# Kernel tuning notes

Measured on AMD Instinct MI355X. Metric: run time of the kernel, lower is better.

## Reference

```python
import jax, jax.numpy as jnp
import numpy as np

N, E, IN, H, K = 50000, 800000, 64, 64, 16


def _linear_params(key, fan_in, fan_out):
    kw, kb = jax.random.split(key)
    lim = 1.0 / np.sqrt(fan_in)
    W = jax.random.uniform(kw, (fan_in, fan_out), jnp.float32, -lim, lim)
    b = jax.random.uniform(kb, (fan_out,), jnp.float32, -lim, lim)
    return W, b


def setup_inputs() -> dict:
    key = jax.random.key(0)
    ks = jax.random.split(key, 16)
    x = jax.random.normal(ks[0], (N, IN), jnp.float32)
    edge_index = jax.random.randint(ks[1], (2, E), 0, N, jnp.int64)
    edge_attr = jax.random.uniform(ks[2], (E, 1), jnp.float32)
    curr_idx = jax.random.randint(ks[3], (), 0, N, jnp.int64)
    dest_idx = jax.random.randint(ks[4], (), 0, N, jnp.int64)
    neighbor_indices = jax.random.randint(ks[5], (K,), 0, N, jnp.int64)
    # GINEConv1 params: edge lift Linear(1->IN), mlp1 Linear(IN->H), Linear(H->H)
    We1, be1 = _linear_params(ks[6], 1, IN)
    W1a, b1a = _linear_params(ks[7], IN, H)
    W1b, b1b = _linear_params(ks[8], H, H)
    # GINEConv2 params: edge lift Linear(1->H), mlp2 Linear(H->H), Linear(H->H)
    We2, be2 = _linear_params(ks[9], 1, H)
    W2a, b2a = _linear_params(ks[10], H, H)
    W2b, b2b = _linear_params(ks[11], H, H)
    # Q head: lin1 Linear(3H->H), lin2 Linear(H->1)
    Wl1, bl1 = _linear_params(ks[12], 3 * H, H)
    Wl2, bl2 = _linear_params(ks[13], H, 1)
    return dict(x=x, edge_index=edge_index, curr_idx=curr_idx, dest_idx=dest_idx,
                neighbor_indices=neighbor_indices, edge_attr=edge_attr,
                We1=We1, be1=be1, W1a=W1a, b1a=b1a, W1b=W1b, b1b=b1b,
                We2=We2, be2=be2, W2a=W2a, b2a=b2a, W2b=W2b, b2b=b2b,
                Wl1=Wl1, bl1=bl1, Wl2=Wl2, bl2=bl2)


def _gine(x, src, dst, e_emb, Wa, ba, Wb, bb):
    # message = ReLU(x_j + edge_emb); aggregate = sum over incoming edges; eps = 0
    msg = jax.nn.relu(x[src] + e_emb)                      # [E, d]
    agg = jax.ops.segment_sum(msg, dst, num_segments=x.shape[0])  # [N, d]
    h = x + agg                                            # (1+eps)*x + agg
    return jax.nn.relu(h @ Wa + ba) @ Wb + bb


def reference(x, edge_index, curr_idx, dest_idx, neighbor_indices, edge_attr,
              We1, be1, W1a, b1a, W1b, b1b,
              We2, be2, W2a, b2a, W2b, b2b,
              Wl1, bl1, Wl2, bl2):
    src, dst = edge_index[0], edge_index[1]
    h = _gine(x, src, dst, edge_attr @ We1 + be1, W1a, b1a, W1b, b1b)
    h = jax.nn.relu(h)
    h = _gine(h, src, dst, edge_attr @ We2 + be2, W2a, b2a, W2b, b2b)  # [N, H]
    curr = h[curr_idx]                 # [H]
    dest = h[dest_idx]                 # [H]
    nbr = h[neighbor_indices]          # [K, H]
    k = nbr.shape[0]
    cat = jnp.concatenate([jnp.broadcast_to(curr, (k, curr.shape[0])),
                           jnp.broadcast_to(dest, (k, dest.shape[0])),
                           nbr], axis=-1)                  # [K, 3H]
    q = jax.nn.relu(cat @ Wl1 + bl1) @ Wl2 + bl2           # [K, 1]
    return q[:, 0]
```

## Files before the change

kernel.cpp:

```cpp
#include <hip/hip_runtime.h>

#define NDIM 64
#define KNBR 16
#define NT 18
#define CAP_S1 1024
#define CAP_B1 128
#define CAP_B2 128

#define OFF_CNT   0
#define OFF_BC1   64
#define OFF_BC2   (OFF_BC1 + CAP_S1*4)
#define OFF_BM    (OFF_BC2 + 128)
#define ZERO_BYTES (OFF_BM + 2048*4)
#define OFF_TGT   ZERO_BYTES
#define OFF_S1    (OFF_TGT + 128)
#define OFF_B1    (OFF_S1 + CAP_S1*4)
#define OFF_B2    (OFF_B1 + CAP_S1*CAP_B1*4)
#define OFF_H     (OFF_B2 + 32*CAP_B2*4)
#define OFF_OUTH  (OFF_H + CAP_S1*NDIM*4)
#define OFF_SLOT  (OFF_OUTH + 32*NDIM*4)

__device__ __forceinline__ int imin(int a, int b) { return a < b ? a : b; }

__device__ __forceinline__ void claim_node(int v, int* slotOf, int* cnt,
                                           int* s1list, unsigned* bm) {
    int prev = atomicCAS(&slotOf[v], -1, -2);
    if (prev == -1) {
        int s = atomicAdd(&cnt[0], 1);
        if (s < CAP_S1) s1list[s] = v;
        __threadfence();
        slotOf[v] = s;
        atomicOr(&bm[v >> 5], 1u << (v & 31));
    }
}

__global__ void k_pass1(const int* __restrict__ src, const int* __restrict__ dst, int E,
                        const int* __restrict__ curr, const int* __restrict__ dest,
                        const int* __restrict__ nbr,
                        int* cnt, int* slotOf, int* s1list, unsigned* bm,
                        int* bc2, int* b2, int* tgt) {
    int t[NT];
    t[0] = curr[0];
    t[1] = dest[0];
    #pragma unroll
    for (int j = 0; j < KNBR; ++j) t[2 + j] = nbr[j];

    if (blockIdx.x == 0 && threadIdx.x < NT) {
        int id = t[threadIdx.x];
        tgt[threadIdx.x] = id;
        claim_node(id, slotOf, cnt, s1list, bm);
    }

    int i = blockIdx.x * blockDim.x + threadIdx.x;
    int e0 = i * 4;
    if (e0 >= E) return;
    int dv4[4];
    if (e0 + 3 < E) {
        int4 dv = ((const int4*)dst)[i];
        dv4[0] = dv.x; dv4[1] = dv.y; dv4[2] = dv.z; dv4[3] = dv.w;
    } else {
        #pragma unroll
        for (int j = 0; j < 4; ++j) dv4[j] = (e0 + j < E) ? dst[e0 + j] : -1;
    }
    #pragma unroll
    for (int j = 0; j < 4; ++j) {
        int d = dv4[j];
        bool any = false;
        #pragma unroll
        for (int k = 0; k < NT; ++k) {
            if (d == t[k]) {
                any = true;
                int idx = atomicAdd(&bc2[k], 1);
                if (idx < CAP_B2) b2[k * CAP_B2 + idx] = e0 + j;
            }
        }
        if (any) claim_node(src[e0 + j], slotOf, cnt, s1list, bm);
    }
}

__global__ void k_pass2(const int* __restrict__ dst, int E,
                        const unsigned* __restrict__ bm, const int* __restrict__ slotOf,
                        int* bc1, int* b1) {
    int i = blockIdx.x * blockDim.x + threadIdx.x;
    int e0 = i * 4;
    if (e0 >= E) return;
    int dv4[4];
    if (e0 + 3 < E) {
        int4 dv = ((const int4*)dst)[i];
        dv4[0] = dv.x; dv4[1] = dv.y; dv4[2] = dv.z; dv4[3] = dv.w;
    } else {
        #pragma unroll
        for (int j = 0; j < 4; ++j) dv4[j] = (e0 + j < E) ? dst[e0 + j] : -1;
    }
    #pragma unroll
    for (int j = 0; j < 4; ++j) {
        int d = dv4[j];
        if (d < 0) continue;
        if ((bm[d >> 5] >> (d & 31)) & 1u) {
            int s = slotOf[d];
            if (s >= 0 && s < CAP_S1) {
                int idx = atomicAdd(&bc1[s], 1);
                if (idx < CAP_B1) b1[s * CAP_B1 + idx] = e0 + j;
            }
        }
    }
}

__global__ void k_node1(const int* cnt, const int* __restrict__ s1list,
                        const int* __restrict__ bc1, const int* __restrict__ b1,
                        const int* __restrict__ src, const float* __restrict__ eattr,
                        const float* __restrict__ x,
                        const float* __restrict__ We1, const float* __restrict__ be1,
                        const float* __restrict__ W1a, const float* __restrict__ b1a,
                        const float* __restrict__ W1b, const float* __restrict__ b1b,
                        float* hbuf) {
    int s = blockIdx.x;
    if (s >= imin(cnt[0], CAP_S1)) return;
    int lane = threadIdx.x;
    __shared__ int   sv[CAP_B1];
    __shared__ float sa[CAP_B1];
    __shared__ float t[NDIM], u[NDIM];
    int m = imin(bc1[s], CAP_B1);
    for (int base = 0; base < m; base += NDIM) {
        int i = base + lane;
        if (i < m) {
            int e = b1[s * CAP_B1 + i];
            sv[i] = src[e];
            sa[i] = eattr[e];
        }
    }
    __syncthreads();
    float w = We1[lane], b = be1[lane];
    int v = s1list[s];
    float acc = x[(size_t)v * NDIM + lane];
    #pragma unroll 4
    for (int i = 0; i < m; ++i)
        acc += fmaxf(x[(size_t)sv[i] * NDIM + lane] + fmaf(sa[i], w, b), 0.f);
    t[lane] = acc;
    __syncthreads();
    float a1 = b1a[lane];
    #pragma unroll
    for (int k = 0; k < NDIM; ++k) a1 = fmaf(t[k], W1a[k * NDIM + lane], a1);
    u[lane] = fmaxf(a1, 0.f);
    __syncthreads();
    float a2 = b1b[lane];
    #pragma unroll
    for (int k = 0; k < NDIM; ++k) a2 = fmaf(u[k], W1b[k * NDIM + lane], a2);
    hbuf[(size_t)s * NDIM + lane] = fmaxf(a2, 0.f);
}

__global__ void k_mlp2(const int* __restrict__ tgt, const int* __restrict__ slotOf,
                       const int* __restrict__ bc2, const int* __restrict__ b2,
                       const int* __restrict__ src, const float* __restrict__ eattr,
                       const float* __restrict__ hbuf,
                       const float* __restrict__ We2, const float* __restrict__ be2,
                       const float* __restrict__ W2a, const float* __restrict__ b2a,
                       const float* __restrict__ W2b, const float* __restrict__ b2b,
                       float* outh) {
    int k = blockIdx.x;
    int lane = threadIdx.x;
    __shared__ int   ss[CAP_B2];
    __shared__ float sa[CAP_B2];
    __shared__ float t[NDIM], u[NDIM];
    int m = imin(bc2[k], CAP_B2);
    for (int base = 0; base < m; base += NDIM) {
        int i = base + lane;
        if (i < m) {
            int e = b2[k * CAP_B2 + i];
            ss[i] = slotOf[src[e]];
            sa[i] = eattr[e];
        }
    }
    __syncthreads();
    int sv = slotOf[tgt[k]];
    float acc = hbuf[(size_t)sv * NDIM + lane];
    float w2e = We2[lane], b2e = be2[lane];
    #pragma unroll 4
    for (int i = 0; i < m; ++i) {
        int s = ss[i];
        if (s >= 0 && s < CAP_S1)
            acc += fmaxf(hbuf[(size_t)s * NDIM + lane] + fmaf(sa[i], w2e, b2e), 0.f);
    }
    t[lane] = acc;
    __syncthreads();
    float a1 = b2a[lane];
    #pragma unroll
    for (int kk = 0; kk < NDIM; ++kk) a1 = fmaf(t[kk], W2a[kk * NDIM + lane], a1);
    u[lane] = fmaxf(a1, 0.f);
    __syncthreads();
    float a2 = b2b[lane];
    #pragma unroll
    for (int kk = 0; kk < NDIM; ++kk) a2 = fmaf(u[kk], W2b[kk * NDIM + lane], a2);
    outh[k * NDIM + lane] = a2;
}

__global__ void k_q(const float* __restrict__ outh,
                    const float* __restrict__ Wl1, const float* __restrict__ bl1,
                    const float* __restrict__ Wl2, const float* __restrict__ bl2,
                    float* out) {
    int j = blockIdx.x;
    int d = threadIdx.x;
    const float* c0 = outh;
    const float* c1 = outh + NDIM;
    const float* cn = outh + (2 + j) * NDIM;
    float acc = bl1[d];
    #pragma unroll
    for (int i = 0; i < NDIM; ++i) acc = fmaf(c0[i], Wl1[i * NDIM + d], acc);
    #pragma unroll
    for (int i = 0; i < NDIM; ++i) acc = fmaf(c1[i], Wl1[(NDIM + i) * NDIM + d], acc);
    #pragma unroll
    for (int i = 0; i < NDIM; ++i) acc = fmaf(cn[i], Wl1[(2 * NDIM + i) * NDIM + d], acc);
    acc = fmaxf(acc, 0.f) * Wl2[d];
    #pragma unroll
    for (int off = 32; off > 0; off >>= 1) acc += __shfl_down(acc, off);
    if (d == 0) out[j] = acc + bl2[0];
}

extern "C" void kernel_launch(void* const* d_in, const int* in_sizes, int n_in,
                              void* d_out, int out_size, void* d_ws, size_t ws_size,
                              hipStream_t stream) {
    const float* x     = (const float*)d_in[0];
    const int*   eidx  = (const int*)d_in[1];
    const int    E     = in_sizes[1] / 2;
    const int    Nn    = in_sizes[0] / NDIM;
    const int*   src   = eidx;
    const int*   dstA  = eidx + E;
    const int*   curr  = (const int*)d_in[2];
    const int*   dest  = (const int*)d_in[3];
    const int*   nbr   = (const int*)d_in[4];
    const float* eattr = (const float*)d_in[5];
    const float* We1 = (const float*)d_in[6];
    const float* be1 = (const float*)d_in[7];
    const float* W1a = (const float*)d_in[8];
    const float* b1a = (const float*)d_in[9];
    const float* W1b = (const float*)d_in[10];
    const float* b1b = (const float*)d_in[11];
    const float* We2 = (const float*)d_in[12];
    const float* be2 = (const float*)d_in[13];
    const float* W2a = (const float*)d_in[14];
    const float* b2a = (const float*)d_in[15];
    const float* W2b = (const float*)d_in[16];
    const float* b2b = (const float*)d_in[17];
    const float* Wl1 = (const float*)d_in[18];
    const float* bl1 = (const float*)d_in[19];
    const float* Wl2 = (const float*)d_in[20];
    const float* bl2 = (const float*)d_in[21];

    char* ws = (char*)d_ws;
    int*      cnt    = (int*)(ws + OFF_CNT);
    int*      bc1    = (int*)(ws + OFF_BC1);
    int*      bc2    = (int*)(ws + OFF_BC2);
    unsigned* bm     = (unsigned*)(ws + OFF_BM);
    int*      tgt    = (int*)(ws + OFF_TGT);
    int*      s1list = (int*)(ws + OFF_S1);
    int*      b1     = (int*)(ws + OFF_B1);
    int*      b2     = (int*)(ws + OFF_B2);
    float*    hbuf   = (float*)(ws + OFF_H);
    float*    outh   = (float*)(ws + OFF_OUTH);
    int*      slotOf = (int*)(ws + OFF_SLOT);

    hipMemsetAsync(ws, 0, ZERO_BYTES, stream);
    hipMemsetAsync(ws + OFF_SLOT, 0xFF, (size_t)Nn * 4, stream);

    int nQuad = (E + 3) / 4;
    int scanBlocks = (nQuad + 255) / 256;

    k_pass1<<<scanBlocks, 256, 0, stream>>>(src, dstA, E, curr, dest, nbr,
                                            cnt, slotOf, s1list, bm, bc2, b2, tgt);
    k_pass2<<<scanBlocks, 256, 0, stream>>>(dstA, E, bm, slotOf, bc1, b1);
    k_node1<<<CAP_S1, NDIM, 0, stream>>>(cnt, s1list, bc1, b1, src, eattr, x,
                                         We1, be1, W1a, b1a, W1b, b1b, hbuf);
    k_mlp2 <<<NT, NDIM, 0, stream>>>(tgt, slotOf, bc2, b2, src, eattr, hbuf,
                                     We2, be2, W2a, b2a, W2b, b2b, outh);
    k_q    <<<KNBR, NDIM, 0, stream>>>(outh, Wl1, bl1, Wl2, bl2, (float*)d_out);
}
```

Baseline: 151.2 us.

## Fuse all stages into one persistent kernel with software grid barriers

Replaces five kernel launches and two memsets with a single persistent kernel of 512 blocks that separates stages with atomic-counter grid barriers. Workspace initialisation moves into the kernel, and the destination indices are loaded once into registers and reused for both edge-scan passes instead of being read from memory twice. Node MLP work is mapped one wave per node, packing four nodes per block. The cost is a spin-wait barrier that assumes all 512 blocks are co-resident, and the final stages run on only a few blocks while the rest sit idle at barriers.

```diff
diff --git a/kernel.cpp b/kernel.cpp
--- a/kernel.cpp
+++ b/kernel.cpp
@@ -6,21 +6,35 @@
 #define CAP_S1 1024
 #define CAP_B1 128
 #define CAP_B2 128
-
-#define OFF_CNT   0
-#define OFF_BC1   64
-#define OFF_BC2   (OFF_BC1 + CAP_S1*4)
-#define OFF_BM    (OFF_BC2 + 128)
-#define ZERO_BYTES (OFF_BM + 2048*4)
-#define OFF_TGT   ZERO_BYTES
-#define OFF_S1    (OFF_TGT + 128)
-#define OFF_B1    (OFF_S1 + CAP_S1*4)
-#define OFF_B2    (OFF_B1 + CAP_S1*CAP_B1*4)
-#define OFF_H     (OFF_B2 + 32*CAP_B2*4)
-#define OFF_OUTH  (OFF_H + CAP_S1*NDIM*4)
-#define OFF_SLOT  (OFF_OUTH + 32*NDIM*4)
+#define GRID 512
+#define TPB 256
+#define MAXJ 8
+
+#define OFF_BAR  0
+#define OFF_CNT  64
+#define OFF_BC1  128
+#define OFF_BC2  (OFF_BC1 + CAP_S1*4)
+#define OFF_BM   (OFF_BC2 + 128)
+#define OFF_TGT  (OFF_BM + 2048*4)
+#define OFF_S1   (OFF_TGT + 128)
+#define OFF_B1   (OFF_S1 + CAP_S1*4)
+#define OFF_B2   (OFF_B1 + CAP_S1*CAP_B1*4)
+#define OFF_H    (OFF_B2 + 32*CAP_B2*4)
+#define OFF_OUTH (OFF_H + CAP_S1*NDIM*4)
+#define OFF_SLOT (OFF_OUTH + 32*NDIM*4)
 
 __device__ __forceinline__ int imin(int a, int b) { return a < b ? a : b; }
+
+__device__ __forceinline__ void gsync(int* bar, int phase) {
+    __syncthreads();
+    if (threadIdx.x == 0) {
+        __threadfence();
+        atomicAdd(&bar[phase], 1);
+        while (atomicAdd(&bar[phase], 0) < GRID) __builtin_amdgcn_s_sleep(1);
+        __threadfence();
+    }
+    __syncthreads();
+}
 
 __device__ __forceinline__ void claim_node(int v, int* slotOf, int* cnt,
                                            int* s1list, unsigned* bm) {
@@ -34,186 +48,182 @@
     }
 }
 
-__global__ void k_pass1(const int* __restrict__ src, const int* __restrict__ dst, int E,
-                        const int* __restrict__ curr, const int* __restrict__ dest,
-                        const int* __restrict__ nbr,
-                        int* cnt, int* slotOf, int* s1list, unsigned* bm,
-                        int* bc2, int* b2, int* tgt) {
-    int t[NT];
-    t[0] = curr[0];
-    t[1] = dest[0];
-    #pragma unroll
-    for (int j = 0; j < KNBR; ++j) t[2 + j] = nbr[j];
-
+extern "C" __global__ void __launch_bounds__(TPB, 4)
+k_fused(const float* __restrict__ x, const int* __restrict__ src,
+        const int* __restrict__ dst, int E, int Nn,
+        const int* __restrict__ curr, const int* __restrict__ dest,
+        const int* __restrict__ nbr, const float* __restrict__ eattr,
+        const float* __restrict__ We1, const float* __restrict__ be1,
+        const float* __restrict__ W1a, const float* __restrict__ b1a,
+        const float* __restrict__ W1b, const float* __restrict__ b1b,
+        const float* __restrict__ We2, const float* __restrict__ be2,
+        const float* __restrict__ W2a, const float* __restrict__ b2a,
+        const float* __restrict__ W2b, const float* __restrict__ b2b,
+        const float* __restrict__ Wl1, const float* __restrict__ bl1,
+        const float* __restrict__ Wl2, const float* __restrict__ bl2,
+        float* __restrict__ out, char* __restrict__ ws) {
+    int*      bar    = (int*)(ws + OFF_BAR);
+    int*      cnt    = (int*)(ws + OFF_CNT);
+    int*      bc1    = (int*)(ws + OFF_BC1);
+    int*      bc2    = (int*)(ws + OFF_BC2);
+    unsigned* bm     = (unsigned*)(ws + OFF_BM);
+    int*      tgt    = (int*)(ws + OFF_TGT);
+    int*      s1list = (int*)(ws + OFF_S1);
+    int*      b1     = (int*)(ws + OFF_B1);
+    int*      b2     = (int*)(ws + OFF_B2);
+    float*    hbuf   = (float*)(ws + OFF_H);
+    float*    outh   = (float*)(ws + OFF_OUTH);
+    int*      slotOf = (int*)(ws + OFF_SLOT);
+
+    const int nthr = GRID * TPB;
+    const int gtid = blockIdx.x * TPB + threadIdx.x;
+    const int wid  = threadIdx.x >> 6;
+    const int lane = threadIdx.x & 63;
+
+    __shared__ int   s_iv[4][CAP_B1];
+    __shared__ float s_fv[4][CAP_B1];
+    __shared__ float s_t[4][NDIM];
+    __shared__ float s_u[4][NDIM];
+
+    for (int i = gtid; i < Nn; i += nthr) slotOf[i] = -1;
+    if (gtid < 2048) bm[gtid] = 0u;
+    if (gtid < CAP_S1) bc1[gtid] = 0;
+    if (gtid < 32) bc2[gtid] = 0;
+    if (gtid < 16) cnt[gtid] = 0;
+    gsync(bar, 0);
+
+    int t0[NT];
+    t0[0] = curr[0];
+    t0[1] = dest[0];
+    #pragma unroll
+    for (int j = 0; j < KNBR; ++j) t0[2 + j] = nbr[j];
     if (blockIdx.x == 0 && threadIdx.x < NT) {
-        int id = t[threadIdx.x];
-        tgt[threadIdx.x] = id;
-        claim_node(id, slotOf, cnt, s1list, bm);
-    }
-
-    int i = blockIdx.x * blockDim.x + threadIdx.x;
-    int e0 = i * 4;
-    if (e0 >= E) return;
-    int dv4[4];
-    if (e0 + 3 < E) {
-        int4 dv = ((const int4*)dst)[i];
-        dv4[0] = dv.x; dv4[1] = dv.y; dv4[2] = dv.z; dv4[3] = dv.w;
-    } else {
-        #pragma unroll
-        for (int j = 0; j < 4; ++j) dv4[j] = (e0 + j < E) ? dst[e0 + j] : -1;
-    }
-    #pragma unroll
-    for (int j = 0; j < 4; ++j) {
-        int d = dv4[j];
+        tgt[threadIdx.x] = t0[threadIdx.x];
+        claim_node(t0[threadIdx.x], slotOf, cnt, s1list, bm);
+    }
+    const int EPT = (E + nthr - 1) / nthr;
+    const int cbase = blockIdx.x * (TPB * EPT);
+    int dv[MAXJ];
+    #pragma unroll
+    for (int j = 0; j < MAXJ; ++j) {
+        int e = cbase + j * TPB + threadIdx.x;
+        dv[j] = (j < EPT && e < E) ? dst[e] : -1;
+    }
+    #pragma unroll
+    for (int j = 0; j < MAXJ; ++j) {
+        int dd = dv[j];
+        if (dd < 0) continue;
+        int e = cbase + j * TPB + threadIdx.x;
         bool any = false;
         #pragma unroll
         for (int k = 0; k < NT; ++k) {
-            if (d == t[k]) {
+            if (dd == t0[k]) {
                 any = true;
                 int idx = atomicAdd(&bc2[k], 1);
-                if (idx < CAP_B2) b2[k * CAP_B2 + idx] = e0 + j;
-            }
-        }
-        if (any) claim_node(src[e0 + j], slotOf, cnt, s1list, bm);
-    }
-}
-
-__global__ void k_pass2(const int* __restrict__ dst, int E,
-                        const unsigned* __restrict__ bm, const int* __restrict__ slotOf,
-                        int* bc1, int* b1) {
-    int i = blockIdx.x * blockDim.x + threadIdx.x;
-    int e0 = i * 4;
-    if (e0 >= E) return;
-    int dv4[4];
-    if (e0 + 3 < E) {
-        int4 dv = ((const int4*)dst)[i];
-        dv4[0] = dv.x; dv4[1] = dv.y; dv4[2] = dv.z; dv4[3] = dv.w;
-    } else {
-        #pragma unroll
-        for (int j = 0; j < 4; ++j) dv4[j] = (e0 + j < E) ? dst[e0 + j] : -1;
-    }
-    #pragma unroll
-    for (int j = 0; j < 4; ++j) {
-        int d = dv4[j];
-        if (d < 0) continue;
-        if ((bm[d >> 5] >> (d & 31)) & 1u) {
-            int s = slotOf[d];
+                if (idx < CAP_B2) b2[k * CAP_B2 + idx] = e;
+            }
+        }
+        if (any) claim_node(src[e], slotOf, cnt, s1list, bm);
+    }
+    gsync(bar, 1);
+
+    #pragma unroll
+    for (int j = 0; j < MAXJ; ++j) {
+        int dd = dv[j];
+        if (dd < 0) continue;
+        if ((bm[dd >> 5] >> (dd & 31)) & 1u) {
+            int s = slotOf[dd];
             if (s >= 0 && s < CAP_S1) {
                 int idx = atomicAdd(&bc1[s], 1);
-                if (idx < CAP_B1) b1[s * CAP_B1 + idx] = e0 + j;
-            }
-        }
-    }
-}
-
-__global__ void k_node1(const int* cnt, const int* __restrict__ s1list,
-                        const int* __restrict__ bc1, const int* __restrict__ b1,
-                        const int* __restrict__ src, const float* __restrict__ eattr,
-                        const float* __restrict__ x,
-                        const float* __restrict__ We1, const float* __restrict__ be1,
-                        const float* __restrict__ W1a, const float* __restrict__ b1a,
-                        const float* __restrict__ W1b, const float* __restrict__ b1b,
-                        float* hbuf) {
-    int s = blockIdx.x;
-    if (s >= imin(cnt[0], CAP_S1)) return;
-    int lane = threadIdx.x;
-    __shared__ int   sv[CAP_B1];
-    __shared__ float sa[CAP_B1];
-    __shared__ float t[NDIM], u[NDIM];
-    int m = imin(bc1[s], CAP_B1);
-    for (int base = 0; base < m; base += NDIM) {
-        int i = base + lane;
-        if (i < m) {
-            int e = b1[s * CAP_B1 + i];
-            sv[i] = src[e];
-            sa[i] = eattr[e];
-        }
-    }
-    __syncthreads();
-    float w = We1[lane], b = be1[lane];
-    int v = s1list[s];
-    float acc = x[(size_t)v * NDIM + lane];
-    #pragma unroll 4
-    for (int i = 0; i < m; ++i)
-        acc += fmaxf(x[(size_t)sv[i] * NDIM + lane] + fmaf(sa[i], w, b), 0.f);
-    t[lane] = acc;
-    __syncthreads();
-    float a1 = b1a[lane];
-    #pragma unroll
-    for (int k = 0; k < NDIM; ++k) a1 = fmaf(t[k], W1a[k * NDIM + lane], a1);
-    u[lane] = fmaxf(a1, 0.f);
-    __syncthreads();
-    float a2 = b1b[lane];
-    #pragma unroll
-    for (int k = 0; k < NDIM; ++k) a2 = fmaf(u[k], W1b[k * NDIM + lane], a2);
-    hbuf[(size_t)s * NDIM + lane] = fmaxf(a2, 0.f);
-}
-
-__global__ void k_mlp2(const int* __restrict__ tgt, const int* __restrict__ slotOf,
-                       const int* __restrict__ bc2, const int* __restrict__ b2,
-                       const int* __restrict__ src, const float* __restrict__ eattr,
-                       const float* __restrict__ hbuf,
-                       const float* __restrict__ We2, const float* __restrict__ be2,
-                       const float* __restrict__ W2a, const float* __restrict__ b2a,
-                       const float* __restrict__ W2b, const float* __restrict__ b2b,
-                       float* outh) {
-    int k = blockIdx.x;
-    int lane = threadIdx.x;
-    __shared__ int   ss[CAP_B2];
-    __shared__ float sa[CAP_B2];
-    __shared__ float t[NDIM], u[NDIM];
-    int m = imin(bc2[k], CAP_B2);
-    for (int base = 0; base < m; base += NDIM) {
-        int i = base + lane;
-        if (i < m) {
-            int e = b2[k * CAP_B2 + i];
-            ss[i] = slotOf[src[e]];
-            sa[i] = eattr[e];
-        }
-    }
-    __syncthreads();
-    int sv = slotOf[tgt[k]];
-    float acc = hbuf[(size_t)sv * NDIM + lane];
-    float w2e = We2[lane], b2e = be2[lane];
-    #pragma unroll 4
-    for (int i = 0; i < m; ++i) {
-        int s = ss[i];
-        if (s >= 0 && s < CAP_S1)
-            acc += fmaxf(hbuf[(size_t)s * NDIM + lane] + fmaf(sa[i], w2e, b2e), 0.f);
-    }
-    t[lane] = acc;
-    __syncthreads();
-    float a1 = b2a[lane];
-    #pragma unroll
-    for (int kk = 0; kk < NDIM; ++kk) a1 = fmaf(t[kk], W2a[kk * NDIM + lane], a1);
-    u[lane] = fmaxf(a1, 0.f);
-    __syncthreads();
-    float a2 = b2b[lane];
-    #pragma unroll
-    for (int kk = 0; kk < NDIM; ++kk) a2 = fmaf(u[kk], W2b[kk * NDIM + lane], a2);
-    outh[k * NDIM + lane] = a2;
-}
-
-__global__ void k_q(const float* __restrict__ outh,
-                    const float* __restrict__ Wl1, const float* __restrict__ bl1,
-                    const float* __restrict__ Wl2, const float* __restrict__ bl2,
-                    float* out) {
-    int j = blockIdx.x;
-    int d = threadIdx.x;
-    const float* c0 = outh;
-    const float* c1 = outh + NDIM;
-    const float* cn = outh + (2 + j) * NDIM;
-    float acc = bl1[d];
-    #pragma unroll
-    for (int i = 0; i < NDIM; ++i) acc = fmaf(c0[i], Wl1[i * NDIM + d], acc);
-    #pragma unroll
-    for (int i = 0; i < NDIM; ++i) acc = fmaf(c1[i], Wl1[(NDIM + i) * NDIM + d], acc);
-    #pragma unroll
-    for (int i = 0; i < NDIM; ++i) acc = fmaf(cn[i], Wl1[(2 * NDIM + i) * NDIM + d], acc);
-    acc = fmaxf(acc, 0.f) * Wl2[d];
-    #pragma unroll
-    for (int off = 32; off > 0; off >>= 1) acc += __shfl_down(acc, off);
-    if (d == 0) out[j] = acc + bl2[0];
+                if (idx < CAP_B1) b1[s * CAP_B1 + idx] = cbase + j * TPB + threadIdx.x;
+            }
+        }
+    }
+    gsync(bar, 2);
+
+    {
+        int nS1 = imin(cnt[0], CAP_S1);
+        int s = blockIdx.x * 4 + wid;
+        if (s < nS1) {
+            int m = imin(bc1[s], CAP_B1);
+            for (int i = lane; i < m; i += 64) {
+                int e = b1[s * CAP_B1 + i];
+                s_iv[wid][i] = src[e];
+                s_fv[wid][i] = eattr[e];
+            }
+            __builtin_amdgcn_wave_barrier();
+            float w = We1[lane], b = be1[lane];
+            int v = s1list[s];
+            float acc = x[(size_t)v * NDIM + lane];
+            for (int i = 0; i < m; ++i)
+                acc += fmaxf(x[(size_t)s_iv[wid][i] * NDIM + lane] + fmaf(s_fv[wid][i], w, b), 0.f);
+            s_t[wid][lane] = acc;
+            __builtin_amdgcn_wave_barrier();
+            float a1 = b1a[lane];
+            #pragma unroll 8
+            for (int k = 0; k < NDIM; ++k) a1 = fmaf(s_t[wid][k], W1a[k * NDIM + lane], a1);
+            s_u[wid][lane] = fmaxf(a1, 0.f);
+            __builtin_amdgcn_wave_barrier();
+            float a2 = b1b[lane];
+            #pragma unroll 8
+            for (int k = 0; k < NDIM; ++k) a2 = fmaf(s_u[wid][k], W1b[k * NDIM + lane], a2);
+            hbuf[(size_t)s * NDIM + lane] = fmaxf(a2, 0.f);
+        }
+    }
+    gsync(bar, 3);
+
+    if (blockIdx.x >= 256 && blockIdx.x < 261) {
+        int k = (blockIdx.x - 256) * 4 + wid;
+        if (k < NT) {
+            int m = imin(bc2[k], CAP_B2);
+            for (int i = lane; i < m; i += 64) {
+                int e = b2[k * CAP_B2 + i];
+                s_iv[wid][i] = slotOf[src[e]];
+                s_fv[wid][i] = eattr[e];
+            }
+            __builtin_amdgcn_wave_barrier();
+            int sv = slotOf[tgt[k]];
+            float acc = hbuf[(size_t)sv * NDIM + lane];
+            float w2e = We2[lane], b2e = be2[lane];
+            for (int i = 0; i < m; ++i) {
+                int s = s_iv[wid][i];
+                if (s >= 0 && s < CAP_S1)
+                    acc += fmaxf(hbuf[(size_t)s * NDIM + lane] + fmaf(s_fv[wid][i], w2e, b2e), 0.f);
+            }
+            s_t[wid][lane] = acc;
+            __builtin_amdgcn_wave_barrier();
+            float a1 = b2a[lane];
+            #pragma unroll 8
+            for (int kk = 0; kk < NDIM; ++kk) a1 = fmaf(s_t[wid][kk], W2a[kk * NDIM + lane], a1);
+            s_u[wid][lane] = fmaxf(a1, 0.f);
+            __builtin_amdgcn_wave_barrier();
+            float a2 = b2b[lane];
+            #pragma unroll 8
+            for (int kk = 0; kk < NDIM; ++kk) a2 = fmaf(s_u[wid][kk], W2b[kk * NDIM + lane], a2);
+            outh[k * NDIM + lane] = a2;
+        }
+    }
+    gsync(bar, 4);
+
+    if (blockIdx.x >= 261 && blockIdx.x < 265) {
+        int j = (blockIdx.x - 261) * 4 + wid;
+        if (j < KNBR) {
+            const float* c0 = outh;
+            const float* c1 = outh + NDIM;
+            const float* cn = outh + (2 + j) * NDIM;
+            float acc = bl1[lane];
+            #pragma unroll 8
+            for (int i = 0; i < NDIM; ++i) acc = fmaf(c0[i], Wl1[i * NDIM + lane], acc);
+            #pragma unroll 8
+            for (int i = 0; i < NDIM; ++i) acc = fmaf(c1[i], Wl1[(NDIM + i) * NDIM + lane], acc);
+            #pragma unroll 8
+            for (int i = 0; i < NDIM; ++i) acc = fmaf(cn[i], Wl1[(2 * NDIM + i) * NDIM + lane], acc);
+            acc = fmaxf(acc, 0.f) * Wl2[lane];
+            #pragma unroll
+            for (int off = 32; off > 0; off >>= 1) acc += __shfl_down(acc, off);
+            if (lane == 0) out[j] = acc + bl2[0];
+        }
+    }
 }
 
 extern "C" void kernel_launch(void* const* d_in, const int* in_sizes, int n_in,
@@ -247,30 +257,12 @@
     const float* bl2 = (const float*)d_in[21];
 
     char* ws = (char*)d_ws;
-    int*      cnt    = (int*)(ws + OFF_CNT);
-    int*      bc1    = (int*)(ws + OFF_BC1);
-    int*      bc2    = (int*)(ws + OFF_BC2);
-    unsigned* bm     = (unsigned*)(ws + OFF_BM);
-    int*      tgt    = (int*)(ws + OFF_TGT);
-    int*      s1list = (int*)(ws + OFF_S1);
-    int*      b1     = (int*)(ws + OFF_B1);
-    int*      b2     = (int*)(ws + OFF_B2);
-    float*    hbuf   = (float*)(ws + OFF_H);
-    float*    outh   = (float*)(ws + OFF_OUTH);
-    int*      slotOf = (int*)(ws + OFF_SLOT);
-
-    hipMemsetAsync(ws, 0, ZERO_BYTES, stream);
-    hipMemsetAsync(ws + OFF_SLOT, 0xFF, (size_t)Nn * 4, stream);
-
-    int nQuad = (E + 3) / 4;
-    int scanBlocks = (nQuad + 255) / 256;
-
-    k_pass1<<<scanBlocks, 256, 0, stream>>>(src, dstA, E, curr, dest, nbr,
-                                            cnt, slotOf, s1list, bm, bc2, b2, tgt);
-    k_pass2<<<scanBlocks, 256, 0, stream>>>(dstA, E, bm, slotOf, bc1, b1);
-    k_node1<<<CAP_S1, NDIM, 0, stream>>>(cnt, s1list, bc1, b1, src, eattr, x,
-                                         We1, be1, W1a, b1a, W1b, b1b, hbuf);
-    k_mlp2 <<<NT, NDIM, 0, stream>>>(tgt, slotOf, bc2, b2, src, eattr, hbuf,
-                                     We2, be2, W2a, b2a, W2b, b2b, outh);
-    k_q    <<<KNBR, NDIM, 0, stream>>>(outh, Wl1, bl1, Wl2, bl2, (float*)d_out);
-}
+
+    hipMemsetAsync(ws + OFF_BAR, 0, 64, stream);
+
+    k_fused<<<GRID, TPB, 0, stream>>>(x, src, dstA, E, Nn, curr, dest, nbr, eattr,
+                                      We1, be1, W1a, b1a, W1b, b1b,
+                                      We2, be2, W2a, b2a, W2b, b2b,
+                                      Wl1, bl1, Wl2, bl2,
+                                      (float*)d_out, ws);
+}
```

Measured after the change: 366.6 us. 142% more time.
